# Kernel tuning notes

Hardware: AMD Instinct MI355X
Metric: run time of the kernel (lower is better)

Reference implementation:

```python
import jax, jax.numpy as jnp
import numpy as np
import math

NUM_POINTS = 9
DILATION = 1
STRIDE = 1
BN_EPS = 1e-5


def _initial_offsets(p):
    g = int(math.ceil(math.sqrt(p)))
    c = (g - 1) / 2.0
    offs = [[i - c, j - c] for i in range(g) for j in range(g)][:p]
    return jnp.asarray(offs, dtype=jnp.float32)  # [P,2] = (dy, dx)


def _bilinear_sample(x, sy, sx):
    # x: [B,C,H,W]; sy, sx: [B,H,W,P] float pixel coords.
    # Zero padding for out-of-bounds corners (matches grid_sample zeros + align_corners=True).
    B, C, H, W = x.shape
    y0 = jnp.floor(sy); x0 = jnp.floor(sx)
    y1 = y0 + 1.0;      x1 = x0 + 1.0
    wy1 = sy - y0; wy0 = 1.0 - wy1
    wx1 = sx - x0; wx0 = 1.0 - wx1
    xf = x.reshape(B, C, H * W)

    def gather(yi, xi):
        valid = ((yi >= 0) & (yi < H) & (xi >= 0) & (xi < W)).astype(x.dtype)
        yc = jnp.clip(yi, 0, H - 1).astype(jnp.int32)
        xc = jnp.clip(xi, 0, W - 1).astype(jnp.int32)
        idx = (yc * W + xc).reshape(B, 1, -1)              # [B,1,H*W*P]
        v = jnp.take_along_axis(xf, idx, axis=2)           # [B,C,H*W*P]
        return v * valid.reshape(B, 1, -1)

    out = (gather(y0, x0) * (wy0 * wx0).reshape(B, 1, -1)
         + gather(y0, x1) * (wy0 * wx1).reshape(B, 1, -1)
         + gather(y1, x0) * (wy1 * wx0).reshape(B, 1, -1)
         + gather(y1, x1) * (wy1 * wx1).reshape(B, 1, -1))
    return out  # [B,C,H*W*P]


def _akconv(x, dw_w, dw_b, bn_gamma, bn_beta, bn_mean, bn_var, pw_w, pw_b, weight, bias):
    B, C, H, W = x.shape
    P = NUM_POINTS
    # offset branch: depthwise 3x3 conv -> BN (eval mode) -> SiLU -> 1x1 conv
    h = jax.lax.conv_general_dilated(x, dw_w, (1, 1), ((1, 1), (1, 1)),
                                     dimension_numbers=('NCHW', 'OIHW', 'NCHW'),
                                     feature_group_count=C)
    h = h + dw_b[None, :, None, None]
    inv = jax.lax.rsqrt(bn_var + BN_EPS)
    h = (h - bn_mean[None, :, None, None]) * (bn_gamma * inv)[None, :, None, None] + bn_beta[None, :, None, None]
    h = h * jax.nn.sigmoid(h)  # SiLU
    off = jax.lax.conv_general_dilated(h, pw_w, (1, 1), ((0, 0), (0, 0)),
                                       dimension_numbers=('NCHW', 'OIHW', 'NCHW'))
    off = off + pw_b[None, :, None, None]                       # [B,2P,H,W]
    off = off.reshape(B, P, 2, H, W).transpose(0, 3, 4, 1, 2)   # [B,H,W,P,2]
    off = (off + _initial_offsets(P)[None, None, None]) * DILATION
    gy = jnp.arange(H, dtype=x.dtype)[None, :, None, None]
    gx = jnp.arange(W, dtype=x.dtype)[None, None, :, None]
    sy = gy + off[..., 0]                                       # [B,H,W,P]
    sx = gx + off[..., 1]
    # (normalize-to-[-1,1] then grid_sample(align_corners=True) cancels exactly -> sample at pixel coords)
    sampled = _bilinear_sample(x, sy, sx).reshape(B, C, H * W, P)
    out = jnp.einsum('bcnp,ocp->bno', sampled, weight) + bias   # [B,HW,O]
    out = out.reshape(B, H, W, -1).transpose(0, 3, 1, 2)        # [B,O,H,W]
    if STRIDE > 1:
        out = out[:, :, ::STRIDE, ::STRIDE]
    return out


def setup_inputs() -> dict:
    key = jax.random.key(0)
    ks = jax.random.split(key, 8)
    B, C, O, H, W, P = 8, 64, 64, 128, 128, NUM_POINTS
    x = jax.random.normal(ks[0], (B, C, H, W), dtype=jnp.float32)
    dw_w = jax.random.normal(ks[1], (C, 1, 3, 3), dtype=jnp.float32) * 0.1
    dw_b = jax.random.normal(ks[2], (C,), dtype=jnp.float32) * 0.05
    bn_gamma = jnp.ones((C,), dtype=jnp.float32)
    bn_beta = jnp.zeros((C,), dtype=jnp.float32)
    bn_mean = jnp.zeros((C,), dtype=jnp.float32)
    bn_var = jnp.ones((C,), dtype=jnp.float32)
    pw_w = jax.random.normal(ks[3], (2 * P, C, 1, 1), dtype=jnp.float32) * 0.01
    pw_b = jnp.zeros((2 * P,), dtype=jnp.float32)
    weight = jax.random.normal(ks[4], (O, C, P), dtype=jnp.float32) * 0.05
    bias = jax.random.normal(ks[5], (O,), dtype=jnp.float32) * 0.05
    return {"x": x, "dw_w": dw_w, "dw_b": dw_b, "bn_gamma": bn_gamma, "bn_beta": bn_beta,
            "bn_mean": bn_mean, "bn_var": bn_var, "pw_w": pw_w, "pw_b": pw_b,
            "weight": weight, "bias": bias}


def reference(x, dw_w, dw_b, bn_gamma, bn_beta, bn_mean, bn_var, pw_w, pw_b, weight, bias):
    return _akconv(x, dw_w, dw_b, bn_gamma, bn_beta, bn_mean, bn_var, pw_w, pw_b, weight, bias)
```

## Files before the change

kernel.cpp:

```cpp
#include <hip/hip_runtime.h>
#include <math.h>

#define BB 8
#define CC 64
#define OO 64
#define HH 128
#define WW 128
#define PP 9
#define HWIMG 16384
#define NTOT  131072
#define RSTR 144

typedef __attribute__((ext_vector_type(8))) _Float16 h8;
typedef __attribute__((ext_vector_type(2))) _Float16 h2;
typedef __attribute__((ext_vector_type(4))) float f32x4;

__global__ void k_prep(const float* __restrict__ w,
                       const float* __restrict__ dw_w,
                       const float* __restrict__ dw_b,
                       const float* __restrict__ gamma,
                       const float* __restrict__ beta,
                       const float* __restrict__ mean,
                       const float* __restrict__ var,
                       const float* __restrict__ pw_w,
                       const float* __restrict__ pw_b,
                       _Float16* __restrict__ wtf2,
                       float* __restrict__ dwt,
                       float* __restrict__ bnA,
                       float* __restrict__ bnB,
                       _Float16* __restrict__ pwa,
                       float* __restrict__ pwb) {
  int bid = blockIdx.x, t = threadIdx.x;
  if (bid < 144) {
    int i = bid * 256 + t;
    int e  = i & 7;
    int ln = (i >> 3) & 63;
    int kc = (i >> 9) & 1;
    int mt = (i >> 10) & 3;
    int p  = i >> 12;
    int o = mt * 16 + (ln & 15);
    int c = kc * 32 + (ln >> 4) * 8 + e;
    wtf2[i] = (_Float16)w[(o * 64 + c) * 9 + p];
  } else {
    if (t < 64) {
      float A = gamma[t] * rsqrtf(var[t] + 1e-5f);
      bnA[t] = A;
      bnB[t] = (dw_b[t] - mean[t]) * A + beta[t];
    }
    if (t < 32) pwb[t] = (t < 18) ? pw_b[t] : 0.f;
    for (int i = t; i < 576; i += 256) {
      int tap = i % 9, c = i / 9;
      dwt[tap * 64 + c] = dw_w[c * 9 + tap];
    }
    for (int i = t; i < 2048; i += 256) {
      int e  = i & 7;
      int ln = (i >> 3) & 63;
      int kc = (i >> 9) & 1;
      int mt = (i >> 10) & 1;
      int ko = mt * 16 + (ln & 15);
      int c  = kc * 32 + ((ln >> 4) & 3) * 8 + e;
      pwa[i] = (ko < 18) ? (_Float16)pw_w[ko * 64 + c] : (_Float16)0.f;
    }
  }
}

__global__ void __launch_bounds__(256, 4)
k_tr(const float* __restrict__ x, _Float16* __restrict__ xt) {
  __shared__ _Float16 lt[64][66];
  int bid = blockIdx.x;
  int vbid = (bid & 7) * 256 + (bid >> 3);
  int tid = threadIdx.x;
  int wid = tid >> 6, ln = tid & 63;
  int b = vbid >> 8;
  int pix0 = (vbid & 255) * 64;
  const float* xbb = x + (size_t)b * CC * HWIMG;

  #pragma unroll
  for (int i = 0; i < 8; ++i) {
    int c0 = (wid * 8 + i) * 2;
    float v0 = xbb[(size_t)c0 * HWIMG + pix0 + ln];
    float v1 = xbb[(size_t)(c0 + 1) * HWIMG + pix0 + ln];
    h2 hv;
    hv[0] = (_Float16)v0;
    hv[1] = (_Float16)v1;
    *(h2*)&lt[ln][c0] = hv;
  }
  __syncthreads();

  int pq = tid >> 2, q = tid & 3;
  h8 o0, o1;
  #pragma unroll
  for (int j = 0; j < 4; ++j) {
    h2 v = *(h2*)&lt[pq][q * 16 + 2 * j];
    o0[2 * j] = v[0];
    o0[2 * j + 1] = v[1];
  }
  #pragma unroll
  for (int j = 0; j < 4; ++j) {
    h2 v = *(h2*)&lt[pq][q * 16 + 8 + 2 * j];
    o1[2 * j] = v[0];
    o1[2 * j + 1] = v[1];
  }
  _Float16* op = xt + ((size_t)((b << 14) + pix0 + pq)) * 64 + q * 16;
  *(h8*)op = o0;
  *(h8*)(op + 8) = o1;
}

template<bool BORDER>
__device__ __forceinline__ void tile_body(
    const _Float16* __restrict__ xb,
    const float* __restrict__ dwt,
    const float* __restrict__ bnA,
    const float* __restrict__ bnB,
    const _Float16* __restrict__ pwa,
    const float* __restrict__ pwb,
    const _Float16* __restrict__ wtf2,
    const float* __restrict__ bias,
    float* __restrict__ out,
    char* smem, int b, int ty0, int tx0, int tid) {
  int wid = tid >> 6, ln = tid & 63;
  int lm = ln & 15, lk = ln >> 4;

  for (int ch = tid; ch < 1920; ch += 256) {
    int rec = ch >> 3, j = ch & 7;
    int ry = rec / 20, rx = rec - ry * 20;
    int yy = min(max(ty0 - 2 + ry, 0), HH - 1);
    int xx = min(max(tx0 - 2 + rx, 0), WW - 1);
    h8 v = *((const h8*)(xb + ((size_t)((yy << 7) + xx)) * 64) + j);
    *(h8*)(smem + rec * RSTR + j * 16) = v;
  }
  __syncthreads();

  int qy0 = wid * 2;
  int y0r = ty0 + qy0;

  float s[2][16];
  #pragma unroll
  for (int nt = 0; nt < 2; ++nt)
    #pragma unroll
    for (int e = 0; e < 16; ++e) s[nt][e] = 0.f;

  #pragma unroll
  for (int tap = 0; tap < 9; ++tap) {
    int dy = tap / 3 - 1, dx = tap % 3 - 1;
    int xc2 = tx0 + lm + dx;
    bool cok = (xc2 >= 0) & (xc2 < WW);
    const float* dwp = dwt + tap * 64;
    f32x4 d0a = *(const f32x4*)(dwp + lk * 8);
    f32x4 d0b = *(const f32x4*)(dwp + lk * 8 + 4);
    f32x4 d1a = *(const f32x4*)(dwp + 32 + lk * 8);
    f32x4 d1b = *(const f32x4*)(dwp + 32 + lk * 8 + 4);
    #pragma unroll
    for (int nt = 0; nt < 2; ++nt) {
      int rec = (qy0 + nt + dy + 2) * 20 + (lm + dx + 2);
      h8 v0 = *(const h8*)(smem + rec * RSTR + (lk    ) * 16);
      h8 v1 = *(const h8*)(smem + rec * RSTR + (lk + 4) * 16);
      if (BORDER) {
        int ry = y0r + nt + dy;
        bool ok = cok & (ry >= 0) & (ry < HH);
        if (!ok) { v0 = (h8)(_Float16)0.f; v1 = (h8)(_Float16)0.f; }
      }
      #pragma unroll
      for (int e = 0; e < 4; ++e) {
        s[nt][e]      += d0a[e] * (float)v0[e];
        s[nt][4 + e]  += d0b[e] * (float)v0[4 + e];
        s[nt][8 + e]  += d1a[e] * (float)v1[e];
        s[nt][12 + e] += d1b[e] * (float)v1[4 + e];
      }
    }
  }

  h8 bo[2][2];
  {
    f32x4 ba0 = *(const f32x4*)(bnA + lk * 8);
    f32x4 ba1 = *(const f32x4*)(bnA + lk * 8 + 4);
    f32x4 ba2 = *(const f32x4*)(bnA + 32 + lk * 8);
    f32x4 ba3 = *(const f32x4*)(bnA + 32 + lk * 8 + 4);
    f32x4 bb0 = *(const f32x4*)(bnB + lk * 8);
    f32x4 bb1 = *(const f32x4*)(bnB + lk * 8 + 4);
    f32x4 bb2 = *(const f32x4*)(bnB + 32 + lk * 8);
    f32x4 bb3 = *(const f32x4*)(bnB + 32 + lk * 8 + 4);
    #pragma unroll
    for (int nt = 0; nt < 2; ++nt) {
      #pragma unroll
      for (int e = 0; e < 4; ++e) {
        float v;
        v = s[nt][e]      * ba0[e] + bb0[e];
        s[nt][e]      = v * __builtin_amdgcn_rcpf(1.f + __expf(-v));
        v = s[nt][4 + e]  * ba1[e] + bb1[e];
        s[nt][4 + e]  = v * __builtin_amdgcn_rcpf(1.f + __expf(-v));
        v = s[nt][8 + e]  * ba2[e] + bb2[e];
        s[nt][8 + e]  = v * __builtin_amdgcn_rcpf(1.f + __expf(-v));
        v = s[nt][12 + e] * ba3[e] + bb3[e];
        s[nt][12 + e] = v * __builtin_amdgcn_rcpf(1.f + __expf(-v));
      }
      #pragma unroll
      for (int e = 0; e < 8; ++e) {
        bo[nt][0][e] = (_Float16)s[nt][e];
        bo[nt][1][e] = (_Float16)s[nt][8 + e];
      }
    }
  }

  f32x4 aco[2][2];
  {
    f32x4 c0 = *(const f32x4*)(pwb + lk * 4);
    f32x4 c1 = *(const f32x4*)(pwb + 16 + lk * 4);
    aco[0][0] = c0; aco[0][1] = c0;
    aco[1][0] = c1; aco[1][1] = c1;
  }
  #pragma unroll
  for (int kc = 0; kc < 2; ++kc) {
    #pragma unroll
    for (int mt = 0; mt < 2; ++mt) {
      h8 A = *(const h8*)(pwa + (mt * 2 + kc) * 512 + ln * 8);
      #pragma unroll
      for (int nt = 0; nt < 2; ++nt)
        aco[mt][nt] = __builtin_amdgcn_mfma_f32_16x16x32_f16(A, bo[nt][kc], aco[mt][nt], 0, 0, 0);
    }
  }

  unsigned pk0[2], pk1[2], pk2[2];
  #pragma unroll
  for (int nt = 0; nt < 2; ++nt) {
    h2 a, b2, c;
    a[0]  = (_Float16)aco[0][nt][0]; a[1]  = (_Float16)aco[0][nt][1];
    b2[0] = (_Float16)aco[0][nt][2]; b2[1] = (_Float16)aco[0][nt][3];
    c[0]  = (_Float16)aco[1][nt][0]; c[1]  = (_Float16)aco[1][nt][1];
    pk0[nt] = __builtin_bit_cast(unsigned, a);
    pk1[nt] = __builtin_bit_cast(unsigned, b2);
    pk2[nt] = __builtin_bit_cast(unsigned, c);
  }

  unsigned ov[2][9];
  #pragma unroll
  for (int nt = 0; nt < 2; ++nt) {
    ov[nt][0] = __shfl(pk0[nt], 0 * 16 + lm);
    ov[nt][1] = __shfl(pk1[nt], 0 * 16 + lm);
    ov[nt][2] = __shfl(pk0[nt], 1 * 16 + lm);
    ov[nt][3] = __shfl(pk1[nt], 1 * 16 + lm);
    ov[nt][4] = __shfl(pk0[nt], 2 * 16 + lm);
    ov[nt][5] = __shfl(pk1[nt], 2 * 16 + lm);
    ov[nt][6] = __shfl(pk0[nt], 3 * 16 + lm);
    ov[nt][7] = __shfl(pk1[nt], 3 * 16 + lm);
    ov[nt][8] = __shfl(pk2[nt], lm);
  }

  f32x4 acc[4][2];
  #pragma unroll
  for (int mt = 0; mt < 4; ++mt)
    #pragma unroll
    for (int nt = 0; nt < 2; ++nt) acc[mt][nt] = (f32x4){0.f, 0.f, 0.f, 0.f};

  const _Float16* wl = wtf2 + ln * 8;

  #pragma unroll
  for (int p = 0; p < PP; ++p) {
    h8 bfr[2][2];
    #pragma unroll
    for (int nt = 0; nt < 2; ++nt) {
      h2 hh = __builtin_bit_cast(h2, ov[nt][p]);
      float sy = (float)hh[0] + (float)(y0r + nt + p / 3 - 1);
      float sx = (float)hh[1] + (float)(tx0 + lm + p % 3 - 1);

      float y0f = floorf(sy), x0f = floorf(sx);
      float wy1 = sy - y0f, wy0 = 1.f - wy1;
      float wx1 = sx - x0f, wx0 = 1.f - wx1;
      int y0 = (int)y0f, x0i = (int)x0f;

      float w00, w01, w10, w11;
      int r00, r01, r10, r11;
      if (BORDER) {
        bool vy0 = (y0 >= 0) & (y0 < HH);
        bool vy1 = (y0 + 1 >= 0) & (y0 + 1 < HH);
        bool vx0 = (x0i >= 0) & (x0i < WW);
        bool vx1 = (x0i + 1 >= 0) & (x0i + 1 < WW);
        w00 = (vy0 && vx0) ? wy0 * wx0 : 0.f;
        w01 = (vy0 && vx1) ? wy0 * wx1 : 0.f;
        w10 = (vy1 && vx0) ? wy1 * wx0 : 0.f;
        w11 = (vy1 && vx1) ? wy1 * wx1 : 0.f;
        int iy0 = min(max(y0 - ty0 + 2, 0), 11);
        int iy1 = min(max(y0 + 1 - ty0 + 2, 0), 11);
        int ix0 = min(max(x0i - tx0 + 2, 0), 19);
        int ix1 = min(max(x0i + 1 - tx0 + 2, 0), 19);
        r00 = iy0 * 20 + ix0; r01 = iy0 * 20 + ix1;
        r10 = iy1 * 20 + ix0; r11 = iy1 * 20 + ix1;
      } else {
        w00 = wy0 * wx0; w01 = wy0 * wx1;
        w10 = wy1 * wx0; w11 = wy1 * wx1;
        int iy0 = y0 - ty0 + 2;
        int ix0 = x0i - tx0 + 2;
        r00 = iy0 * 20 + ix0; r01 = r00 + 1;
        r10 = r00 + 20;       r11 = r00 + 21;
      }

      h8 v00a = *(const h8*)(smem + r00 * RSTR + (lk    ) * 16);
      h8 v00b = *(const h8*)(smem + r00 * RSTR + (lk + 4) * 16);
      h8 v01a = *(const h8*)(smem + r01 * RSTR + (lk    ) * 16);
      h8 v01b = *(const h8*)(smem + r01 * RSTR + (lk + 4) * 16);
      h8 v10a = *(const h8*)(smem + r10 * RSTR + (lk    ) * 16);
      h8 v10b = *(const h8*)(smem + r10 * RSTR + (lk + 4) * 16);
      h8 v11a = *(const h8*)(smem + r11 * RSTR + (lk    ) * 16);
      h8 v11b = *(const h8*)(smem + r11 * RSTR + (lk + 4) * 16);

      h8 w00v = (h8)(_Float16)w00;
      h8 w01v = (h8)(_Float16)w01;
      h8 w10v = (h8)(_Float16)w10;
      h8 w11v = (h8)(_Float16)w11;
      bfr[nt][0] = v00a * w00v + v01a * w01v + v10a * w10v + v11a * w11v;
      bfr[nt][1] = v00b * w00v + v01b * w01v + v10b * w10v + v11b * w11v;
    }

    #pragma unroll
    for (int mt = 0; mt < 4; ++mt) {
      h8 a0 = *(const h8*)(wl + (p * 8 + mt * 2) * 512);
      h8 a1 = *(const h8*)(wl + (p * 8 + mt * 2 + 1) * 512);
      #pragma unroll
      for (int nt = 0; nt < 2; ++nt) {
        acc[mt][nt] = __builtin_amdgcn_mfma_f32_16x16x32_f16(a0, bfr[nt][0], acc[mt][nt], 0, 0, 0);
        acc[mt][nt] = __builtin_amdgcn_mfma_f32_16x16x32_f16(a1, bfr[nt][1], acc[mt][nt], 0, 0, 0);
      }
    }
  }

  #pragma unroll
  for (int nt = 0; nt < 2; ++nt) {
    int pix = ((y0r + nt) << 7) + tx0 + lm;
    #pragma unroll
    for (int mt = 0; mt < 4; ++mt) {
      #pragma unroll
      for (int r = 0; r < 4; ++r) {
        int m = mt * 16 + lk * 4 + r;
        out[((size_t)b * OO + m) * HWIMG + pix] = acc[mt][nt][r] + bias[m];
      }
    }
  }
}

__global__ void __launch_bounds__(256, 4)
k_main(const _Float16* __restrict__ xt,
       const float* __restrict__ dwt,
       const float* __restrict__ bnA,
       const float* __restrict__ bnB,
       const _Float16* __restrict__ pwa,
       const float* __restrict__ pwb,
       const _Float16* __restrict__ wtf2,
       const float* __restrict__ bias,
       float* __restrict__ out) {
  __shared__ __attribute__((aligned(16))) char smem[240 * RSTR];
  int bid = blockIdx.x;
  int b = bid & 7, t = bid >> 3;
  int ty0 = (t >> 3) * 8, tx0 = (t & 7) * 16;
  int tid = threadIdx.x;
  const _Float16* xb = xt + (((size_t)b) << 14) * 64;

  bool border = (ty0 == 0) || (ty0 == 120) || (tx0 == 0) || (tx0 == 112);
  if (border)
    tile_body<true >(xb, dwt, bnA, bnB, pwa, pwb, wtf2, bias, out, smem, b, ty0, tx0, tid);
  else
    tile_body<false>(xb, dwt, bnA, bnB, pwa, pwb, wtf2, bias, out, smem, b, ty0, tx0, tid);
}

extern "C" void kernel_launch(void* const* d_in, const int* in_sizes, int n_in,
                              void* d_out, int out_size, void* d_ws, size_t ws_size,
                              hipStream_t stream) {
  const float* x        = (const float*)d_in[0];
  const float* dw_w     = (const float*)d_in[1];
  const float* dw_b     = (const float*)d_in[2];
  const float* bn_gamma = (const float*)d_in[3];
  const float* bn_beta  = (const float*)d_in[4];
  const float* bn_mean  = (const float*)d_in[5];
  const float* bn_var   = (const float*)d_in[6];
  const float* pw_w     = (const float*)d_in[7];
  const float* pw_b     = (const float*)d_in[8];
  const float* weight   = (const float*)d_in[9];
  const float* bias     = (const float*)d_in[10];
  float* out = (float*)d_out;

  char* ws = (char*)d_ws;
  _Float16* wtf2 = (_Float16*)ws;
  size_t o1 = (size_t)PP * OO * CC * 2;
  _Float16* xtb = (_Float16*)(ws + o1);
  size_t o2 = o1 + (size_t)NTOT * CC * 2;
  float* dwt = (float*)(ws + o2);
  float* bnA = (float*)(ws + o2 + 2304);
  float* bnB = (float*)(ws + o2 + 2304 + 256);
  _Float16* pwa = (_Float16*)(ws + o2 + 2304 + 512);
  float* pwb = (float*)(ws + o2 + 2304 + 512 + 4096);

  k_prep<<<145, 256, 0, stream>>>(weight, dw_w, dw_b, bn_gamma, bn_beta,
                                  bn_mean, bn_var, pw_w, pw_b,
                                  wtf2, dwt, bnA, bnB, pwa, pwb);
  k_tr<<<NTOT / 64, 256, 0, stream>>>(x, xtb);
  k_main<<<NTOT / 128, 256, 0, stream>>>(xtb, dwt, bnA, bnB, pwa, pwb,
                                         wtf2, bias, out);
}
```

Measured before the change: 51.87 us.

## Shrink main tile to 4x16 pixels with one row per wave for occupancy

Each block now covers 4 rows by 16 columns instead of 8 by 16. Each wave handles a single output row, so the two-row nt dimension disappears from the depthwise, offset-MFMA, sampling and output accumulators. The LDS halo shrinks to 160 records, the grid doubles, and launch bounds rise to 6 blocks per CU. This is meant to cut register and LDS pressure and raise occupancy. In exchange, halo reloads per output pixel go up, and weight fragments loaded from global serve half as many MFMAs.

```diff
diff --git a/kernel.cpp b/kernel.cpp
--- a/kernel.cpp
+++ b/kernel.cpp
@@ -121,7 +121,7 @@
   int wid = tid >> 6, ln = tid & 63;
   int lm = ln & 15, lk = ln >> 4;
 
-  for (int ch = tid; ch < 1920; ch += 256) {
+  for (int ch = tid; ch < 1280; ch += 256) {
     int rec = ch >> 3, j = ch & 7;
     int ry = rec / 20, rx = rec - ry * 20;
     int yy = min(max(ty0 - 2 + ry, 0), HH - 1);
@@ -131,46 +131,39 @@
   }
   __syncthreads();
 
-  int qy0 = wid * 2;
-  int y0r = ty0 + qy0;
-
-  float s[2][16];
-  #pragma unroll
-  for (int nt = 0; nt < 2; ++nt)
-    #pragma unroll
-    for (int e = 0; e < 16; ++e) s[nt][e] = 0.f;
+  int row = ty0 + wid;
+
+  float s[16];
+  #pragma unroll
+  for (int e = 0; e < 16; ++e) s[e] = 0.f;
 
   #pragma unroll
   for (int tap = 0; tap < 9; ++tap) {
     int dy = tap / 3 - 1, dx = tap % 3 - 1;
-    int xc2 = tx0 + lm + dx;
-    bool cok = (xc2 >= 0) & (xc2 < WW);
     const float* dwp = dwt + tap * 64;
     f32x4 d0a = *(const f32x4*)(dwp + lk * 8);
     f32x4 d0b = *(const f32x4*)(dwp + lk * 8 + 4);
     f32x4 d1a = *(const f32x4*)(dwp + 32 + lk * 8);
     f32x4 d1b = *(const f32x4*)(dwp + 32 + lk * 8 + 4);
-    #pragma unroll
-    for (int nt = 0; nt < 2; ++nt) {
-      int rec = (qy0 + nt + dy + 2) * 20 + (lm + dx + 2);
-      h8 v0 = *(const h8*)(smem + rec * RSTR + (lk    ) * 16);
-      h8 v1 = *(const h8*)(smem + rec * RSTR + (lk + 4) * 16);
-      if (BORDER) {
-        int ry = y0r + nt + dy;
-        bool ok = cok & (ry >= 0) & (ry < HH);
-        if (!ok) { v0 = (h8)(_Float16)0.f; v1 = (h8)(_Float16)0.f; }
-      }
-      #pragma unroll
-      for (int e = 0; e < 4; ++e) {
-        s[nt][e]      += d0a[e] * (float)v0[e];
-        s[nt][4 + e]  += d0b[e] * (float)v0[4 + e];
-        s[nt][8 + e]  += d1a[e] * (float)v1[e];
-        s[nt][12 + e] += d1b[e] * (float)v1[4 + e];
-      }
-    }
-  }
-
-  h8 bo[2][2];
+    int rec = (wid + dy + 2) * 20 + (lm + dx + 2);
+    h8 v0 = *(const h8*)(smem + rec * RSTR + (lk    ) * 16);
+    h8 v1 = *(const h8*)(smem + rec * RSTR + (lk + 4) * 16);
+    if (BORDER) {
+      int xc2 = tx0 + lm + dx;
+      int ry = row + dy;
+      bool ok = (xc2 >= 0) & (xc2 < WW) & (ry >= 0) & (ry < HH);
+      if (!ok) { v0 = (h8)(_Float16)0.f; v1 = (h8)(_Float16)0.f; }
+    }
+    #pragma unroll
+    for (int e = 0; e < 4; ++e) {
+      s[e]      += d0a[e] * (float)v0[e];
+      s[4 + e]  += d0b[e] * (float)v0[4 + e];
+      s[8 + e]  += d1a[e] * (float)v1[e];
+      s[12 + e] += d1b[e] * (float)v1[4 + e];
+    }
+  }
+
+  h8 bo[2];
   {
     f32x4 ba0 = *(const f32x4*)(bnA + lk * 8);
     f32x4 ba1 = *(const f32x4*)(bnA + lk * 8 + 4);
@@ -181,163 +174,137 @@
     f32x4 bb2 = *(const f32x4*)(bnB + 32 + lk * 8);
     f32x4 bb3 = *(const f32x4*)(bnB + 32 + lk * 8 + 4);
     #pragma unroll
-    for (int nt = 0; nt < 2; ++nt) {
-      #pragma unroll
-      for (int e = 0; e < 4; ++e) {
-        float v;
-        v = s[nt][e]      * ba0[e] + bb0[e];
-        s[nt][e]      = v * __builtin_amdgcn_rcpf(1.f + __expf(-v));
-        v = s[nt][4 + e]  * ba1[e] + bb1[e];
-        s[nt][4 + e]  = v * __builtin_amdgcn_rcpf(1.f + __expf(-v));
-        v = s[nt][8 + e]  * ba2[e] + bb2[e];
-        s[nt][8 + e]  = v * __builtin_amdgcn_rcpf(1.f + __expf(-v));
-        v = s[nt][12 + e] * ba3[e] + bb3[e];
-        s[nt][12 + e] = v * __builtin_amdgcn_rcpf(1.f + __expf(-v));
-      }
-      #pragma unroll
-      for (int e = 0; e < 8; ++e) {
-        bo[nt][0][e] = (_Float16)s[nt][e];
-        bo[nt][1][e] = (_Float16)s[nt][8 + e];
-      }
-    }
-  }
-
-  f32x4 aco[2][2];
-  {
-    f32x4 c0 = *(const f32x4*)(pwb + lk * 4);
-    f32x4 c1 = *(const f32x4*)(pwb + 16 + lk * 4);
-    aco[0][0] = c0; aco[0][1] = c0;
-    aco[1][0] = c1; aco[1][1] = c1;
-  }
+    for (int e = 0; e < 4; ++e) {
+      float v;
+      v = s[e]      * ba0[e] + bb0[e];
+      s[e]      = v * __builtin_amdgcn_rcpf(1.f + __expf(-v));
+      v = s[4 + e]  * ba1[e] + bb1[e];
+      s[4 + e]  = v * __builtin_amdgcn_rcpf(1.f + __expf(-v));
+      v = s[8 + e]  * ba2[e] + bb2[e];
+      s[8 + e]  = v * __builtin_amdgcn_rcpf(1.f + __expf(-v));
+      v = s[12 + e] * ba3[e] + bb3[e];
+      s[12 + e] = v * __builtin_amdgcn_rcpf(1.f + __expf(-v));
+    }
+    #pragma unroll
+    for (int e = 0; e < 8; ++e) {
+      bo[0][e] = (_Float16)s[e];
+      bo[1][e] = (_Float16)s[8 + e];
+    }
+  }
+
+  f32x4 aco[2];
+  aco[0] = *(const f32x4*)(pwb + lk * 4);
+  aco[1] = *(const f32x4*)(pwb + 16 + lk * 4);
   #pragma unroll
   for (int kc = 0; kc < 2; ++kc) {
     #pragma unroll
     for (int mt = 0; mt < 2; ++mt) {
       h8 A = *(const h8*)(pwa + (mt * 2 + kc) * 512 + ln * 8);
-      #pragma unroll
-      for (int nt = 0; nt < 2; ++nt)
-        aco[mt][nt] = __builtin_amdgcn_mfma_f32_16x16x32_f16(A, bo[nt][kc], aco[mt][nt], 0, 0, 0);
-    }
-  }
-
-  unsigned pk0[2], pk1[2], pk2[2];
-  #pragma unroll
-  for (int nt = 0; nt < 2; ++nt) {
+      aco[mt] = __builtin_amdgcn_mfma_f32_16x16x32_f16(A, bo[kc], aco[mt], 0, 0, 0);
+    }
+  }
+
+  unsigned pk0, pk1, pk2;
+  {
     h2 a, b2, c;
-    a[0]  = (_Float16)aco[0][nt][0]; a[1]  = (_Float16)aco[0][nt][1];
-    b2[0] = (_Float16)aco[0][nt][2]; b2[1] = (_Float16)aco[0][nt][3];
-    c[0]  = (_Float16)aco[1][nt][0]; c[1]  = (_Float16)aco[1][nt][1];
-    pk0[nt] = __builtin_bit_cast(unsigned, a);
-    pk1[nt] = __builtin_bit_cast(unsigned, b2);
-    pk2[nt] = __builtin_bit_cast(unsigned, c);
-  }
-
-  unsigned ov[2][9];
-  #pragma unroll
-  for (int nt = 0; nt < 2; ++nt) {
-    ov[nt][0] = __shfl(pk0[nt], 0 * 16 + lm);
-    ov[nt][1] = __shfl(pk1[nt], 0 * 16 + lm);
-    ov[nt][2] = __shfl(pk0[nt], 1 * 16 + lm);
-    ov[nt][3] = __shfl(pk1[nt], 1 * 16 + lm);
-    ov[nt][4] = __shfl(pk0[nt], 2 * 16 + lm);
-    ov[nt][5] = __shfl(pk1[nt], 2 * 16 + lm);
-    ov[nt][6] = __shfl(pk0[nt], 3 * 16 + lm);
-    ov[nt][7] = __shfl(pk1[nt], 3 * 16 + lm);
-    ov[nt][8] = __shfl(pk2[nt], lm);
-  }
-
-  f32x4 acc[4][2];
-  #pragma unroll
-  for (int mt = 0; mt < 4; ++mt)
-    #pragma unroll
-    for (int nt = 0; nt < 2; ++nt) acc[mt][nt] = (f32x4){0.f, 0.f, 0.f, 0.f};
+    a[0]  = (_Float16)aco[0][0]; a[1]  = (_Float16)aco[0][1];
+    b2[0] = (_Float16)aco[0][2]; b2[1] = (_Float16)aco[0][3];
+    c[0]  = (_Float16)aco[1][0]; c[1]  = (_Float16)aco[1][1];
+    pk0 = __builtin_bit_cast(unsigned, a);
+    pk1 = __builtin_bit_cast(unsigned, b2);
+    pk2 = __builtin_bit_cast(unsigned, c);
+  }
+  unsigned ov[9];
+  ov[0] = __shfl(pk0, 0 * 16 + lm);
+  ov[1] = __shfl(pk1, 0 * 16 + lm);
+  ov[2] = __shfl(pk0, 1 * 16 + lm);
+  ov[3] = __shfl(pk1, 1 * 16 + lm);
+  ov[4] = __shfl(pk0, 2 * 16 + lm);
+  ov[5] = __shfl(pk1, 2 * 16 + lm);
+  ov[6] = __shfl(pk0, 3 * 16 + lm);
+  ov[7] = __shfl(pk1, 3 * 16 + lm);
+  ov[8] = __shfl(pk2, lm);
+
+  f32x4 acc[4];
+  #pragma unroll
+  for (int mt = 0; mt < 4; ++mt) acc[mt] = (f32x4){0.f, 0.f, 0.f, 0.f};
 
   const _Float16* wl = wtf2 + ln * 8;
 
   #pragma unroll
   for (int p = 0; p < PP; ++p) {
-    h8 bfr[2][2];
-    #pragma unroll
-    for (int nt = 0; nt < 2; ++nt) {
-      h2 hh = __builtin_bit_cast(h2, ov[nt][p]);
-      float sy = (float)hh[0] + (float)(y0r + nt + p / 3 - 1);
-      float sx = (float)hh[1] + (float)(tx0 + lm + p % 3 - 1);
-
-      float y0f = floorf(sy), x0f = floorf(sx);
-      float wy1 = sy - y0f, wy0 = 1.f - wy1;
-      float wx1 = sx - x0f, wx0 = 1.f - wx1;
-      int y0 = (int)y0f, x0i = (int)x0f;
-
-      float w00, w01, w10, w11;
-      int r00, r01, r10, r11;
-      if (BORDER) {
-        bool vy0 = (y0 >= 0) & (y0 < HH);
-        bool vy1 = (y0 + 1 >= 0) & (y0 + 1 < HH);
-        bool vx0 = (x0i >= 0) & (x0i < WW);
-        bool vx1 = (x0i + 1 >= 0) & (x0i + 1 < WW);
-        w00 = (vy0 && vx0) ? wy0 * wx0 : 0.f;
-        w01 = (vy0 && vx1) ? wy0 * wx1 : 0.f;
-        w10 = (vy1 && vx0) ? wy1 * wx0 : 0.f;
-        w11 = (vy1 && vx1) ? wy1 * wx1 : 0.f;
-        int iy0 = min(max(y0 - ty0 + 2, 0), 11);
-        int iy1 = min(max(y0 + 1 - ty0 + 2, 0), 11);
-        int ix0 = min(max(x0i - tx0 + 2, 0), 19);
-        int ix1 = min(max(x0i + 1 - tx0 + 2, 0), 19);
-        r00 = iy0 * 20 + ix0; r01 = iy0 * 20 + ix1;
-        r10 = iy1 * 20 + ix0; r11 = iy1 * 20 + ix1;
-      } else {
-        w00 = wy0 * wx0; w01 = wy0 * wx1;
-        w10 = wy1 * wx0; w11 = wy1 * wx1;
-        int iy0 = y0 - ty0 + 2;
-        int ix0 = x0i - tx0 + 2;
-        r00 = iy0 * 20 + ix0; r01 = r00 + 1;
-        r10 = r00 + 20;       r11 = r00 + 21;
-      }
-
-      h8 v00a = *(const h8*)(smem + r00 * RSTR + (lk    ) * 16);
-      h8 v00b = *(const h8*)(smem + r00 * RSTR + (lk + 4) * 16);
-      h8 v01a = *(const h8*)(smem + r01 * RSTR + (lk    ) * 16);
-      h8 v01b = *(const h8*)(smem + r01 * RSTR + (lk + 4) * 16);
-      h8 v10a = *(const h8*)(smem + r10 * RSTR + (lk    ) * 16);
-      h8 v10b = *(const h8*)(smem + r10 * RSTR + (lk + 4) * 16);
-      h8 v11a = *(const h8*)(smem + r11 * RSTR + (lk    ) * 16);
-      h8 v11b = *(const h8*)(smem + r11 * RSTR + (lk + 4) * 16);
-
-      h8 w00v = (h8)(_Float16)w00;
-      h8 w01v = (h8)(_Float16)w01;
-      h8 w10v = (h8)(_Float16)w10;
-      h8 w11v = (h8)(_Float16)w11;
-      bfr[nt][0] = v00a * w00v + v01a * w01v + v10a * w10v + v11a * w11v;
-      bfr[nt][1] = v00b * w00v + v01b * w01v + v10b * w10v + v11b * w11v;
-    }
+    h2 hh = __builtin_bit_cast(h2, ov[p]);
+    float sy = (float)hh[0] + (float)(row + p / 3 - 1);
+    float sx = (float)hh[1] + (float)(tx0 + lm + p % 3 - 1);
+
+    float y0f = floorf(sy), x0f = floorf(sx);
+    float wy1 = sy - y0f, wy0 = 1.f - wy1;
+    float wx1 = sx - x0f, wx0 = 1.f - wx1;
+    int y0 = (int)y0f, x0i = (int)x0f;
+
+    float w00, w01, w10, w11;
+    int r00, r01, r10, r11;
+    if (BORDER) {
+      bool vy0 = (y0 >= 0) & (y0 < HH);
+      bool vy1 = (y0 + 1 >= 0) & (y0 + 1 < HH);
+      bool vx0 = (x0i >= 0) & (x0i < WW);
+      bool vx1 = (x0i + 1 >= 0) & (x0i + 1 < WW);
+      w00 = (vy0 && vx0) ? wy0 * wx0 : 0.f;
+      w01 = (vy0 && vx1) ? wy0 * wx1 : 0.f;
+      w10 = (vy1 && vx0) ? wy1 * wx0 : 0.f;
+      w11 = (vy1 && vx1) ? wy1 * wx1 : 0.f;
+      int iy0 = min(max(y0 - ty0 + 2, 0), 7);
+      int iy1 = min(max(y0 + 1 - ty0 + 2, 0), 7);
+      int ix0 = min(max(x0i - tx0 + 2, 0), 19);
+      int ix1 = min(max(x0i + 1 - tx0 + 2, 0), 19);
+      r00 = iy0 * 20 + ix0; r01 = iy0 * 20 + ix1;
+      r10 = iy1 * 20 + ix0; r11 = iy1 * 20 + ix1;
+    } else {
+      w00 = wy0 * wx0; w01 = wy0 * wx1;
+      w10 = wy1 * wx0; w11 = wy1 * wx1;
+      int iy0 = y0 - ty0 + 2;
+      int ix0 = x0i - tx0 + 2;
+      r00 = iy0 * 20 + ix0; r01 = r00 + 1;
+      r10 = r00 + 20;       r11 = r00 + 21;
+    }
+
+    h8 v00a = *(const h8*)(smem + r00 * RSTR + (lk    ) * 16);
+    h8 v00b = *(const h8*)(smem + r00 * RSTR + (lk + 4) * 16);
+    h8 v01a = *(const h8*)(smem + r01 * RSTR + (lk    ) * 16);
+    h8 v01b = *(const h8*)(smem + r01 * RSTR + (lk + 4) * 16);
+    h8 v10a = *(const h8*)(smem + r10 * RSTR + (lk    ) * 16);
+    h8 v10b = *(const h8*)(smem + r10 * RSTR + (lk + 4) * 16);
+    h8 v11a = *(const h8*)(smem + r11 * RSTR + (lk    ) * 16);
+    h8 v11b = *(const h8*)(smem + r11 * RSTR + (lk + 4) * 16);
+
+    h8 w00v = (h8)(_Float16)w00;
+    h8 w01v = (h8)(_Float16)w01;
+    h8 w10v = (h8)(_Float16)w10;
+    h8 w11v = (h8)(_Float16)w11;
+    h8 bf0 = v00a * w00v + v01a * w01v + v10a * w10v + v11a * w11v;
+    h8 bf1 = v00b * w00v + v01b * w01v + v10b * w10v + v11b * w11v;
 
     #pragma unroll
     for (int mt = 0; mt < 4; ++mt) {
       h8 a0 = *(const h8*)(wl + (p * 8 + mt * 2) * 512);
       h8 a1 = *(const h8*)(wl + (p * 8 + mt * 2 + 1) * 512);
-      #pragma unroll
-      for (int nt = 0; nt < 2; ++nt) {
-        acc[mt][nt] = __builtin_amdgcn_mfma_f32_16x16x32_f16(a0, bfr[nt][0], acc[mt][nt], 0, 0, 0);
-        acc[mt][nt] = __builtin_amdgcn_mfma_f32_16x16x32_f16(a1, bfr[nt][1], acc[mt][nt], 0, 0, 0);
-      }
-    }
-  }
-
-  #pragma unroll
-  for (int nt = 0; nt < 2; ++nt) {
-    int pix = ((y0r + nt) << 7) + tx0 + lm;
-    #pragma unroll
-    for (int mt = 0; mt < 4; ++mt) {
-      #pragma unroll
-      for (int r = 0; r < 4; ++r) {
-        int m = mt * 16 + lk * 4 + r;
-        out[((size_t)b * OO + m) * HWIMG + pix] = acc[mt][nt][r] + bias[m];
-      }
-    }
-  }
-}
-
-__global__ void __launch_bounds__(256, 4)
+      acc[mt] = __builtin_amdgcn_mfma_f32_16x16x32_f16(a0, bf0, acc[mt], 0, 0, 0);
+      acc[mt] = __builtin_amdgcn_mfma_f32_16x16x32_f16(a1, bf1, acc[mt], 0, 0, 0);
+    }
+  }
+
+  int pix = (row << 7) + tx0 + lm;
+  #pragma unroll
+  for (int mt = 0; mt < 4; ++mt) {
+    #pragma unroll
+    for (int r = 0; r < 4; ++r) {
+      int m = mt * 16 + lk * 4 + r;
+      out[((size_t)b * OO + m) * HWIMG + pix] = acc[mt][r] + bias[m];
+    }
+  }
+}
+
+__global__ void __launch_bounds__(256, 6)
 k_main(const _Float16* __restrict__ xt,
        const float* __restrict__ dwt,
        const float* __restrict__ bnA,
@@ -347,14 +314,14 @@
        const _Float16* __restrict__ wtf2,
        const float* __restrict__ bias,
        float* __restrict__ out) {
-  __shared__ __attribute__((aligned(16))) char smem[240 * RSTR];
+  __shared__ __attribute__((aligned(16))) char smem[160 * RSTR];
   int bid = blockIdx.x;
   int b = bid & 7, t = bid >> 3;
-  int ty0 = (t >> 3) * 8, tx0 = (t & 7) * 16;
+  int ty0 = (t >> 3) * 4, tx0 = (t & 7) * 16;
   int tid = threadIdx.x;
   const _Float16* xb = xt + (((size_t)b) << 14) * 64;
 
-  bool border = (ty0 == 0) || (ty0 == 120) || (tx0 == 0) || (tx0 == 112);
+  bool border = (ty0 == 0) || (ty0 == 124) || (tx0 == 0) || (tx0 == 112);
   if (border)
     tile_body<true >(xb, dwt, bnA, bnB, pwa, pwb, wtf2, bias, out, smem, b, ty0, tx0, tid);
   else
@@ -392,6 +359,6 @@
                                   bn_mean, bn_var, pw_w, pw_b,
                                   wtf2, dwt, bnA, bnB, pwa, pwb);
   k_tr<<<NTOT / 64, 256, 0, stream>>>(x, xtb);
-  k_main<<<NTOT / 128, 256, 0, stream>>>(xtb, dwt, bnA, bnB, pwa, pwb,
-                                         wtf2, bias, out);
-}
+  k_main<<<NTOT / 64, 256, 0, stream>>>(xtb, dwt, bnA, bnB, pwa, pwb,
+                                        wtf2, bias, out);
+}
```

After: 58.14 us. 12.1% more time.
